# Kernel tuning notes

Hardware: AMD Instinct MI355X
Metric: run time of the kernel (lower is better)

Reference implementation:

```python
import jax, jax.numpy as jnp
import numpy as np

NUM_HEADS = 16


def setup_inputs() -> dict:
    key = jax.random.key(0)
    k1, k2, k3 = jax.random.split(key, 3)
    b, s, d_model = 4, 4096, 1024
    x = jax.random.normal(k1, (b, s, d_model), dtype=jnp.float32)
    w_qkv = jax.random.normal(k2, (3 * d_model, d_model), dtype=jnp.float32) * 0.02
    b_qkv = jnp.zeros((3 * d_model,), dtype=jnp.float32)
    w_out = jax.random.normal(k3, (d_model, d_model), dtype=jnp.float32) * 0.02
    b_out = jnp.zeros((d_model,), dtype=jnp.float32)
    return {"x": x, "w_qkv": w_qkv, "b_qkv": b_qkv, "w_out": w_out, "b_out": b_out}


def reference(x, w_qkv, b_qkv, w_out, b_out):
    b, s, d_model = x.shape
    h = NUM_HEADS
    hd = d_model // h
    # qkv projection: [b, s, 3*d_model]
    qkv = jnp.einsum('bsd,ed->bse', x, w_qkv) + b_qkv
    # rearrange 'b s (three h d) -> three b h s d'
    qkv = qkv.reshape(b, s, 3, h, hd).transpose(2, 0, 3, 1, 4)  # [3, b, h, s, hd]
    q, k, v = qkv[0], qkv[1], qkv[2]
    # elu feature map
    q = jax.nn.elu(q) + 1.0
    k = jax.nn.elu(k) + 1.0
    # kv state: [b, h, hd, hd]
    kv = jnp.einsum('bhsd,bhse->bhde', k, v)
    # output: [b, h, s, hd]
    out = jnp.einsum('bhsd,bhde->bhse', q, kv)
    # normalization (elementwise divide by per-feature k sum, broadcast over s)
    k_sum = k.sum(axis=-2, keepdims=True)  # [b, h, 1, hd]
    out = out / (k_sum + 1e-6)
    # 'b h s d -> b s (h d)'
    out = out.transpose(0, 2, 1, 3).reshape(b, s, d_model)
    return jnp.einsum('bsd,ed->bse', out, w_out) + b_out
```

## Files before the change

kernel.cpp:

```cpp
#include <hip/hip_runtime.h>
#include <stdint.h>

typedef float f32x4 __attribute__((ext_vector_type(4)));
typedef __bf16 bf16x8 __attribute__((ext_vector_type(8)));
typedef unsigned short u16;
typedef u16 u16x8 __attribute__((ext_vector_type(8)));

__device__ __forceinline__ u16 f2bf(float f) {
  uint32_t u = __builtin_bit_cast(uint32_t, f);
  return (u16)((u + 0x7fffu + ((u >> 16) & 1u)) >> 16);
}
__device__ __forceinline__ float bf2f(u16 h) {
  uint32_t u = ((uint32_t)h) << 16;
  return __builtin_bit_cast(float, u);
}
__device__ __forceinline__ float elup1(float x) {
  return x > 0.f ? x + 1.f : __expf(x);
}
__device__ __forceinline__ void gll16(const void* g, void* l) {
  __builtin_amdgcn_global_load_lds(
      (const __attribute__((address_space(1))) unsigned int*)g,
      (__attribute__((address_space(3))) unsigned int*)l, 16, 0, 0);
}

#define BAR() __builtin_amdgcn_s_barrier()
#define VMC(n) asm volatile("s_waitcnt vmcnt(" #n ")" ::: "memory")

__global__ void cvt_kernel(const float* __restrict__ in, u16* __restrict__ out, int n4) {
  int i = blockIdx.x * 256 + threadIdx.x;
  if (i >= n4) return;
  float4 f = ((const float4*)in)[i];
  ushort4 o;
  o.x = f2bf(f.x); o.y = f2bf(f.y); o.z = f2bf(f.z); o.w = f2bf(f.w);
  ((ushort4*)out)[i] = o;
}

template <int EPI>
__global__ __launch_bounds__(512, 2)
void gemm256(const u16* __restrict__ A, const u16* __restrict__ B,
             const float* __restrict__ bias, void* __restrict__ Cout,
             int N, int K, int nbj) {
  __shared__ __align__(16) u16 lds[65536];
  const int tid = threadIdx.x;
  const int wave = tid >> 6, lane = tid & 63;
  const int fr = lane & 15, fq = lane >> 4;
  const int wm = wave >> 2, wn = wave & 3;

  const int nwg = gridDim.x;
  const int cpx = nwg >> 3;
  const int swz = (blockIdx.x & 7) * cpx + (blockIdx.x >> 3);
  const int bi = swz / nbj, bj = swz % nbj;

  const u16* Ab = A + (size_t)bi * 256 * K;
  const u16* Bb = B + (size_t)bj * 256 * K;

  const int l8 = lane >> 3;
  const int cswz = ((lane & 7) ^ l8) << 3;
  const int r6 = wave * 8 + l8;

#define STAGE_A(d, h, k0)                                                      \
  { _Pragma("unroll")                                                          \
    for (int i_ = 0; i_ < 2; ++i_) {                                           \
      int gr_ = i_ * 128 + (h) * 64 + r6;                                      \
      gll16(Ab + (size_t)gr_ * K + (k0) + cswz,                                \
            &lds[((d) * 32768 + (h) * 16384 + i_ * 8192 + wave * 1024) >> 1]); \
    } }

#define STAGE_B(d, h, k0)                                                      \
  { _Pragma("unroll")                                                          \
    for (int i_ = 0; i_ < 2; ++i_) {                                           \
      int r_ = i_ * 64 + r6;                                                   \
      int gr_ = (r_ >> 5) * 64 + (h) * 32 + (r_ & 31);                         \
      gll16(Bb + (size_t)gr_ * K + (k0) + cswz,                                \
            &lds[(65536 + (d) * 32768 + (h) * 16384 + i_ * 8192 + wave * 1024) >> 1]); \
    } }

  const int xorc = (fr & 7) << 4;
  const int acol[2] = {(fq * 16) ^ xorc, (64 + fq * 16) ^ xorc};
  const int arow = (wm * 64 + fr) * 128;
  const int brow = (wn * 32 + fr) * 128;

#define LDSV(off) (*(const bf16x8*)&lds[(off) >> 1])

  f32x4 acc[8][4] = {};
  bf16x8 af[4][2];
  bf16x8 bfr[2][2][2];

#define READ_A(d, mh)                                                          \
  { _Pragma("unroll")                                                          \
    for (int ks = 0; ks < 2; ++ks) {                                           \
      _Pragma("unroll")                                                        \
      for (int mm = 0; mm < 4; ++mm)                                           \
        af[mm][ks] = LDSV((d) * 32768 + (mh) * 16384 + arow + mm * 2048 + acol[ks]); \
    } }

#define READ_B(d, nh)                                                          \
  { _Pragma("unroll")                                                          \
    for (int ks = 0; ks < 2; ++ks) {                                           \
      _Pragma("unroll")                                                        \
      for (int nn = 0; nn < 2; ++nn)                                           \
        bfr[nh][nn][ks] = LDSV(65536 + (d) * 32768 + (nh) * 16384 + brow + nn * 2048 + acol[ks]); \
    } }

#define MFMA_Q(mh, nh)                                                         \
  { __builtin_amdgcn_s_setprio(1);                                             \
    _Pragma("unroll")                                                          \
    for (int ks = 0; ks < 2; ++ks) {                                           \
      _Pragma("unroll")                                                        \
      for (int mm = 0; mm < 4; ++mm) {                                         \
        _Pragma("unroll")                                                      \
        for (int nn = 0; nn < 2; ++nn)                                         \
          acc[(mh) * 4 + mm][(nh) * 2 + nn] = __builtin_amdgcn_mfma_f32_16x16x32_bf16( \
              af[mm][ks], bfr[nh][nn][ks], acc[(mh) * 4 + mm][(nh) * 2 + nn], 0, 0, 0); \
      } }                                                                      \
    __builtin_amdgcn_s_setprio(0); }

  const int NT = K >> 6;
  STAGE_A(0, 0, 0); STAGE_B(0, 0, 0); STAGE_B(0, 1, 0); STAGE_A(0, 1, 0);
  STAGE_A(1, 0, 64); STAGE_B(1, 0, 64); STAGE_B(1, 1, 64);
  VMC(6);
  BAR();

  for (int t = 0; t < NT; ++t) {
    const int d = t & 1;
    const int k1 = (t + 1) << 6, k2 = (t + 2) << 6;
    READ_B(d, 0); READ_A(d, 0);
    if (t + 1 < NT) STAGE_A(d ^ 1, 1, k1);
    MFMA_Q(0, 0);
    READ_B(d, 1);
    MFMA_Q(0, 1);
    BAR();
    READ_A(d, 1);
    if (t + 2 < NT) { STAGE_A(d, 0, k2); STAGE_B(d, 0, k2); }
    MFMA_Q(1, 1);
    if (t + 2 < NT) STAGE_B(d, 1, k2);
    MFMA_Q(1, 0);
    if (t < NT - 2) { VMC(6); } else { VMC(0); }
    BAR();
  }

  const int wrow = wm * 128, wcol = wn * 64;
  if (EPI == 0) {
    const bool do_elu = (bj * 256) < 2048;
    float bv[4];
#pragma unroll
    for (int n = 0; n < 4; ++n) bv[n] = bias[bj * 256 + wcol + n * 16 + fr];
    u16* wbuf = &lds[wave * 8192];
    const int lrow = lane >> 3, lcol = (lane & 7) * 8;
#pragma unroll
    for (int ch = 0; ch < 2; ++ch) {
#pragma unroll
      for (int m2 = 0; m2 < 4; ++m2)
#pragma unroll
        for (int n = 0; n < 4; ++n)
#pragma unroll
          for (int r = 0; r < 4; ++r) {
            float v = acc[ch * 4 + m2][n][r] + bv[n];
            if (do_elu) v = elup1(v);
            wbuf[(m2 * 16 + fq * 4 + r) * 72 + n * 16 + fr] = f2bf(v);
          }
#pragma unroll
      for (int i = 0; i < 8; ++i) {
        bf16x8 val = *(const bf16x8*)&wbuf[(i * 8 + lrow) * 72 + lcol];
        const int rowg = bi * 256 + wrow + ch * 64 + i * 8 + lrow;
        *(bf16x8*)&((u16*)Cout)[(size_t)rowg * N + bj * 256 + wcol + lcol] = val;
      }
    }
  } else {
#pragma unroll
    for (int n = 0; n < 4; ++n) {
      const int colg = bj * 256 + wcol + n * 16 + fr;
      const float bv = bias[colg];
#pragma unroll
      for (int m = 0; m < 8; ++m)
#pragma unroll
        for (int r = 0; r < 4; ++r) {
          const int rowg = bi * 256 + wrow + m * 16 + fq * 4 + r;
          ((float*)Cout)[(size_t)rowg * N + colg] = acc[m][n][r] + bv;
        }
    }
  }
#undef STAGE_A
#undef STAGE_B
#undef READ_A
#undef READ_B
#undef MFMA_Q
#undef LDSV
}

__global__ __launch_bounds__(256)
void kv_state_kernel(const u16* __restrict__ qkv, float* __restrict__ pkv,
                     float* __restrict__ pks) {
  const int bh = blockIdx.x, chunk = blockIdx.y;
  const int b = bh >> 4, h = bh & 15;
  const int t = threadIdx.x;
  __shared__ float sK[16][68];
  __shared__ float sV[16][68];
  const int td = t >> 2;
  const int te = (t & 3) * 16;
  f32x4 acc0 = {}, acc1 = {}, acc2 = {}, acc3 = {};
  float aks = 0.f;
  const size_t rowbase = ((size_t)b * 4096 + (size_t)chunk * 512) * 3072;
  const u16* kp = qkv + rowbase + 1024 + h * 64;
  const u16* vp = qkv + rowbase + 2048 + h * 64;
  const int lhalf = t >> 7, lr = (t >> 3) & 15, lc = (t & 7) * 8;
  const u16* lsrc = lhalf ? vp : kp;
  float* ldst = lhalf ? &sV[lr][lc] : &sK[lr][lc];
  for (int s0 = 0; s0 < 512; s0 += 16) {
    u16x8 v8 = *(const u16x8*)&lsrc[(size_t)(s0 + lr) * 3072 + lc];
#pragma unroll
    for (int j = 0; j < 8; ++j) ldst[j] = bf2f(v8[j]);
    __syncthreads();
#pragma unroll 4
    for (int sl = 0; sl < 16; ++sl) {
      float kd = sK[sl][td];
      if ((t & 3) == 0) aks += kd;
      const f32x4* v4 = (const f32x4*)&sV[sl][te];
      acc0 += kd * v4[0];
      acc1 += kd * v4[1];
      acc2 += kd * v4[2];
      acc3 += kd * v4[3];
    }
    __syncthreads();
  }
  float* outp = pkv + ((size_t)chunk * 64 + bh) * 4096 + td * 64 + te;
  *(f32x4*)(outp + 0) = acc0;
  *(f32x4*)(outp + 4) = acc1;
  *(f32x4*)(outp + 8) = acc2;
  *(f32x4*)(outp + 12) = acc3;
  if ((t & 3) == 0) pks[((size_t)chunk * 64 + bh) * 64 + td] = aks;
}

__global__ __launch_bounds__(256)
void kv_reduce_kernel(const float* __restrict__ pkv, const float* __restrict__ pks,
                      float* __restrict__ kvn) {
  const int bh = blockIdx.x;
  const int t = threadIdx.x;
  __shared__ float sks[64];
  if (t < 64) {
    float s = 0.f;
    for (int c = 0; c < 8; ++c) s += pks[((size_t)c * 64 + bh) * 64 + t];
    sks[t] = s + 1e-6f;
  }
  __syncthreads();
#pragma unroll
  for (int j = 0; j < 16; ++j) {
    int idx = t + j * 256;
    float s = 0.f;
    for (int c = 0; c < 8; ++c) s += pkv[((size_t)c * 64 + bh) * 4096 + idx];
    kvn[(size_t)bh * 4096 + idx] = s / sks[idx & 63];
  }
}

__global__ __launch_bounds__(256)
void attn_out_kernel(const u16* __restrict__ qkv, const float* __restrict__ kvn,
                     u16* __restrict__ attn) {
  const int bh = blockIdx.x;
  const int b = bh >> 4, h = bh & 15;
  const int stile = blockIdx.y;
  const int wave = threadIdx.x >> 6, lane = threadIdx.x & 63;
  const int s0 = stile * 64 + wave * 16;
  const int fr = lane & 15, fq = lane >> 4;
  __shared__ u16 sO[4][16 * 72];
  const float* kv = kvn + (size_t)bh * 4096;
  bf16x8 bfrag[2][4];
#pragma unroll
  for (int ks = 0; ks < 2; ++ks)
#pragma unroll
    for (int n = 0; n < 4; ++n) {
      u16x8 tmp;
#pragma unroll
      for (int j = 0; j < 8; ++j)
        tmp[j] = f2bf(kv[(size_t)(ks * 32 + fq * 8 + j) * 64 + n * 16 + fr]);
      bfrag[ks][n] = __builtin_bit_cast(bf16x8, tmp);
    }
  const u16* q = qkv + (size_t)b * 4096 * 3072 + h * 64;
  f32x4 acc[4] = {};
#pragma unroll
  for (int ks = 0; ks < 2; ++ks) {
    bf16x8 af = *(const bf16x8*)&q[(size_t)(s0 + fr) * 3072 + ks * 32 + fq * 8];
#pragma unroll
    for (int n = 0; n < 4; ++n)
      acc[n] = __builtin_amdgcn_mfma_f32_16x16x32_bf16(af, bfrag[ks][n], acc[n], 0, 0, 0);
  }
  u16* wb = &sO[wave][0];
#pragma unroll
  for (int n = 0; n < 4; ++n)
#pragma unroll
    for (int r = 0; r < 4; ++r)
      wb[(fq * 4 + r) * 72 + n * 16 + fr] = f2bf(acc[n][r]);
  u16* ap = attn + (size_t)b * 4096 * 1024 + h * 64;
  const int lrow = lane >> 3, lcol = (lane & 7) * 8;
#pragma unroll
  for (int i = 0; i < 2; ++i) {
    bf16x8 val = *(const bf16x8*)&wb[(i * 8 + lrow) * 72 + lcol];
    *(bf16x8*)&ap[(size_t)(s0 + i * 8 + lrow) * 1024 + lcol] = val;
  }
}

extern "C" void kernel_launch(void* const* d_in, const int* in_sizes, int n_in,
                              void* d_out, int out_size, void* d_ws, size_t ws_size,
                              hipStream_t stream) {
  const float* x     = (const float*)d_in[0];
  const float* w_qkv = (const float*)d_in[1];
  const float* b_qkv = (const float*)d_in[2];
  const float* w_out = (const float*)d_in[3];
  const float* b_out = (const float*)d_in[4];
  float* out = (float*)d_out;

  const int M = 16384, Dm = 1024, N3 = 3072;

  char* ws = (char*)d_ws;
  u16* xb     = (u16*)(ws);
  u16* wqb    = (u16*)(ws + 33554432);
  u16* wob    = (u16*)(ws + 39845888);
  u16* qkvb   = (u16*)(ws + 41943040);
  u16* attnb  = (u16*)(ws + 142606336);
  float* pkv  = (float*)(ws + 176160768);
  float* pks  = (float*)(ws + 184549376);
  float* kvn  = (float*)(ws + 184680448);

  cvt_kernel<<<(M * Dm / 4 + 255) / 256, 256, 0, stream>>>(x, xb, M * Dm / 4);
  cvt_kernel<<<(N3 * Dm / 4 + 255) / 256, 256, 0, stream>>>(w_qkv, wqb, N3 * Dm / 4);
  cvt_kernel<<<(Dm * Dm / 4 + 255) / 256, 256, 0, stream>>>(w_out, wob, Dm * Dm / 4);

  gemm256<0><<<(M / 256) * (N3 / 256), 512, 0, stream>>>(xb, wqb, b_qkv, qkvb, N3, Dm, N3 / 256);
  kv_state_kernel<<<dim3(64, 8), 256, 0, stream>>>(qkvb, pkv, pks);
  kv_reduce_kernel<<<64, 256, 0, stream>>>(pkv, pks, kvn);
  attn_out_kernel<<<dim3(64, 64), 256, 0, stream>>>(qkvb, kvn, attnb);
  gemm256<1><<<(M / 256) * (Dm / 256), 512, 0, stream>>>(attnb, wob, b_out, out, Dm, Dm, Dm / 256);
}
```

Measured before the change: 264.4 us.

## Merge conversion launches, reorder GEMM staging, re-tile kv_state outer product

```diff
diff --git a/kernel.cpp b/kernel.cpp
--- a/kernel.cpp
+++ b/kernel.cpp
@@ -26,9 +26,19 @@
 #define BAR() __builtin_amdgcn_s_barrier()
 #define VMC(n) asm volatile("s_waitcnt vmcnt(" #n ")" ::: "memory")
 
-__global__ void cvt_kernel(const float* __restrict__ in, u16* __restrict__ out, int n4) {
+__global__ void cvt_all_kernel(const float* __restrict__ x, u16* __restrict__ xb,
+                               const float* __restrict__ wq, u16* __restrict__ wqb,
+                               const float* __restrict__ wo, u16* __restrict__ wob) {
   int i = blockIdx.x * 256 + threadIdx.x;
-  if (i >= n4) return;
+  const float* in;
+  u16* out;
+  if (i < 4194304) {
+    in = x; out = xb;
+  } else if (i < 4980736) {
+    in = wq; out = wqb; i -= 4194304;
+  } else {
+    in = wo; out = wob; i -= 4980736;
+  }
   float4 f = ((const float4*)in)[i];
   ushort4 o;
   o.x = f2bf(f.x); o.y = f2bf(f.y); o.z = f2bf(f.z); o.w = f2bf(f.w);
@@ -124,14 +134,14 @@
   for (int t = 0; t < NT; ++t) {
     const int d = t & 1;
     const int k1 = (t + 1) << 6, k2 = (t + 2) << 6;
+    if (t + 1 < NT) STAGE_A(d ^ 1, 1, k1);
     READ_B(d, 0); READ_A(d, 0);
-    if (t + 1 < NT) STAGE_A(d ^ 1, 1, k1);
     MFMA_Q(0, 0);
     READ_B(d, 1);
     MFMA_Q(0, 1);
     BAR();
+    if (t + 2 < NT) { STAGE_A(d, 0, k2); STAGE_B(d, 0, k2); }
     READ_A(d, 1);
-    if (t + 2 < NT) { STAGE_A(d, 0, k2); STAGE_B(d, 0, k2); }
     MFMA_Q(1, 1);
     if (t + 2 < NT) STAGE_B(d, 1, k2);
     MFMA_Q(1, 0);
@@ -196,10 +206,10 @@
   const int t = threadIdx.x;
   __shared__ float sK[16][68];
   __shared__ float sV[16][68];
-  const int td = t >> 2;
-  const int te = (t & 3) * 16;
+  const int dg = (t & 15) * 4;
+  const int eg = (t >> 4) * 4;
   f32x4 acc0 = {}, acc1 = {}, acc2 = {}, acc3 = {};
-  float aks = 0.f;
+  f32x4 ak4 = {};
   const size_t rowbase = ((size_t)b * 4096 + (size_t)chunk * 512) * 3072;
   const u16* kp = qkv + rowbase + 1024 + h * 64;
   const u16* vp = qkv + rowbase + 2048 + h * 64;
@@ -213,22 +223,22 @@
     __syncthreads();
 #pragma unroll 4
     for (int sl = 0; sl < 16; ++sl) {
-      float kd = sK[sl][td];
-      if ((t & 3) == 0) aks += kd;
-      const f32x4* v4 = (const f32x4*)&sV[sl][te];
-      acc0 += kd * v4[0];
-      acc1 += kd * v4[1];
-      acc2 += kd * v4[2];
-      acc3 += kd * v4[3];
+      const f32x4 kv4 = *(const f32x4*)&sK[sl][dg];
+      const f32x4 vv4 = *(const f32x4*)&sV[sl][eg];
+      acc0 += kv4[0] * vv4;
+      acc1 += kv4[1] * vv4;
+      acc2 += kv4[2] * vv4;
+      acc3 += kv4[3] * vv4;
+      ak4 += kv4;
     }
     __syncthreads();
   }
-  float* outp = pkv + ((size_t)chunk * 64 + bh) * 4096 + td * 64 + te;
-  *(f32x4*)(outp + 0) = acc0;
-  *(f32x4*)(outp + 4) = acc1;
-  *(f32x4*)(outp + 8) = acc2;
-  *(f32x4*)(outp + 12) = acc3;
-  if ((t & 3) == 0) pks[((size_t)chunk * 64 + bh) * 64 + td] = aks;
+  float* outp = pkv + ((size_t)chunk * 64 + bh) * 4096;
+  *(f32x4*)&outp[(dg + 0) * 64 + eg] = acc0;
+  *(f32x4*)&outp[(dg + 1) * 64 + eg] = acc1;
+  *(f32x4*)&outp[(dg + 2) * 64 + eg] = acc2;
+  *(f32x4*)&outp[(dg + 3) * 64 + eg] = acc3;
+  if (t < 16) *(f32x4*)&pks[((size_t)chunk * 64 + bh) * 64 + dg] = ak4;
 }
 
 __global__ __launch_bounds__(256)
@@ -320,9 +330,7 @@
   float* pks  = (float*)(ws + 184549376);
   float* kvn  = (float*)(ws + 184680448);
 
-  cvt_kernel<<<(M * Dm / 4 + 255) / 256, 256, 0, stream>>>(x, xb, M * Dm / 4);
-  cvt_kernel<<<(N3 * Dm / 4 + 255) / 256, 256, 0, stream>>>(w_qkv, wqb, N3 * Dm / 4);
-  cvt_kernel<<<(Dm * Dm / 4 + 255) / 256, 256, 0, stream>>>(w_out, wob, Dm * Dm / 4);
+  cvt_all_kernel<<<20480, 256, 0, stream>>>(x, xb, w_qkv, wqb, w_out, wob);
 
   gemm256<0><<<(M / 256) * (N3 / 256), 512, 0, stream>>>(xb, wqb, b_qkv, qkvb, N3, Dm, N3 / 256);
   kv_state_kernel<<<dim3(64, 8), 256, 0, stream>>>(qkvb, pkv, pks);
```

Measured after the change: 241.7 us. -8.6%, faster.
